# Kernel tuning notes

Hardware: AMD Instinct MI355X
Metric: run time of the kernel (lower is better)

## Reference

```python
import jax, jax.numpy as jnp
import numpy as np


def setup_inputs() -> dict:
    key = jax.random.key(0)
    ks = jax.random.split(key, 6)
    B, C_in, C_out, H, W = 4, 256, 128, 64, 64
    return {
        "p": jax.random.normal(ks[0], (B, C_in, H, W), dtype=jnp.float32),
        "b": jax.random.normal(ks[1], (B, C_in, H, W), dtype=jnp.float32),
        "Wq": jax.random.normal(ks[2], (C_out, C_in), dtype=jnp.float32) * 0.05,
        "bq": jax.random.normal(ks[3], (C_out,), dtype=jnp.float32) * 0.05,
        "Wk": jax.random.normal(ks[4], (C_out, C_in), dtype=jnp.float32) * 0.05,
        "bk": jax.random.normal(ks[5], (C_out,), dtype=jnp.float32) * 0.05,
    }


def reference(p, b, Wq, bq, Wk, bk):
    # p, b: [B, C, H, W]; 1x1 convs are per-pixel GEMMs over channels.
    B, C, H, W = p.shape
    N = H * W
    p_flat = p.reshape(B, C, N)  # [B, C, N]
    b_flat = b.reshape(B, C, N)  # [B, C, N]
    # query = Conv1x1(p) -> [B, O, N] -> permuted to [B, N, O]
    q = jnp.einsum("bcn,oc->bno", p_flat, Wq) + bq  # [B, N, O]
    # key = Conv1x1(b) -> [B, O, N]
    k = jnp.einsum("bcn,oc->bon", b_flat, Wk) + bk[:, None]  # [B, O, N]
    energy = jnp.einsum("bno,bom->bnm", q, k)  # [B, N, N]
    attention = jax.nn.softmax(energy, axis=-1)
    # value = b flattened, attention applied over spatial tokens
    out = jnp.einsum("bnm,bcm->bcn", attention, b_flat)  # [B, C, N]
    return out.reshape(B, C, H, W)
```

## Files before the change

### kernel.cpp

```cpp
#include <hip/hip_runtime.h>
#include <stdint.h>


#define B_ 4
#define C_ 256
#define O_ 128
#define N_ 4096

#define AP 72
#define PP 40

typedef float v4f __attribute__((ext_vector_type(4)));
typedef short v8s __attribute__((ext_vector_type(8)));
typedef _Float16 v8h __attribute__((ext_vector_type(8)));
typedef uint32_t u32;
typedef unsigned short u16;

__device__ __forceinline__ u16 bf16_rne(float f) {
  u32 u = __builtin_bit_cast(u32, f);
  u += 0x7fffu + ((u >> 16) & 1u);
  return (u16)(u >> 16);
}
__device__ __forceinline__ float bf16_f(u16 s) {
  u32 u = ((u32)s) << 16;
  return __builtin_bit_cast(float, u);
}
__device__ __forceinline__ u16 f16_rne(float f) {
  _Float16 h = (_Float16)f;
  return __builtin_bit_cast(u16, h);
}
__device__ __forceinline__ float f16_f(u16 s) {
  return (float)__builtin_bit_cast(_Float16, s);
}
__device__ __forceinline__ v4f mfma16(v8s a, v8s b, v4f c) {
  return __builtin_amdgcn_mfma_f32_16x16x32_bf16(a, b, c, 0, 0, 0);
}
__device__ __forceinline__ v4f mfma16h(v8h a, v8h b, v4f c) {
  return __builtin_amdgcn_mfma_f32_16x16x32_f16(a, b, c, 0, 0, 0);
}
__device__ __forceinline__ void gl16(const u16* g, u16* l) {
  __builtin_amdgcn_global_load_lds(
      (const __attribute__((address_space(1))) u32*)g,
      (__attribute__((address_space(3))) u32*)l, 16, 0, 0);
}
template <int CTRL>
__device__ __forceinline__ float dppadd(float x) {
  int yi = __builtin_amdgcn_update_dpp(0, __builtin_bit_cast(int, x), CTRL,
                                       0xf, 0xf, true);
  return x + __builtin_bit_cast(float, yi);
}
__device__ __forceinline__ float sum16(float x) {
  x = dppadd<0xB1>(x);
  x = dppadd<0x4E>(x);
  x = dppadd<0x141>(x);
  x = dppadd<0x140>(x);
  return x;
}

__global__ __launch_bounds__(256) void k_proj(
    const float* __restrict__ Xp, const float* __restrict__ Wq,
    const float* __restrict__ bq, const float* __restrict__ Xb,
    const float* __restrict__ Wk, const float* __restrict__ bk,
    u16* __restrict__ Qh, u16* __restrict__ Ql, u16* __restrict__ Kh,
    u16* __restrict__ Vbf) {
  __shared__ __align__(16) short ah[64 * AP];
  __shared__ __align__(16) short al[64 * AP];
  __shared__ __align__(16) short wh[128 * AP];
  __shared__ __align__(16) short wl[128 * AP];
  const int tid = threadIdx.x;
  const int inst = blockIdx.x >> 8;
  const float* X = inst ? Xb : Xp;
  const float* W = inst ? Wk : Wq;
  const float* bias = inst ? bk : bq;
  const int b = (blockIdx.x >> 6) & 3;
  const int n0 = (blockIdx.x & 63) << 6;
  const int w = tid >> 6, lane = tid & 63, l15 = lane & 15, quad = lane >> 4;
  v4f acc[8];
#pragma unroll
  for (int t = 0; t < 8; t++) acc[t] = (v4f){0.f, 0.f, 0.f, 0.f};

  for (int c0 = 0; c0 < C_; c0 += 64) {
    __syncthreads();
    {
      const int c = tid >> 2, nch = (tid & 3) << 4;
      const float* s = X + ((size_t)(b * C_ + c0 + c)) * N_ + n0 + nch;
      float4 f0 = ((const float4*)s)[0], f1 = ((const float4*)s)[1],
             f2 = ((const float4*)s)[2], f3 = ((const float4*)s)[3];
      float v[16] = {f0.x, f0.y, f0.z, f0.w, f1.x, f1.y, f1.z, f1.w,
                     f2.x, f2.y, f2.z, f2.w, f3.x, f3.y, f3.z, f3.w};
      u16 hh[16];
#pragma unroll
      for (int j = 0; j < 16; j++) {
        u16 h = bf16_rne(v[j]);
        u16 l = bf16_rne(v[j] - bf16_f(h));
        hh[j] = h;
        ah[(nch + j) * AP + c] = (short)h;
        al[(nch + j) * AP + c] = (short)l;
      }
      if (inst) {
        u32 pk[8];
#pragma unroll
        for (int jj = 0; jj < 8; jj++)
          pk[jj] = (u32)hh[2 * jj] | ((u32)hh[2 * jj + 1] << 16);
        u16* vd = Vbf + ((size_t)(b * C_ + c0 + c)) * N_ + n0 + nch;
        ((uint4*)vd)[0] = make_uint4(pk[0], pk[1], pk[2], pk[3]);
        ((uint4*)vd)[1] = make_uint4(pk[4], pk[5], pk[6], pk[7]);
      }
    }
    {
      const int o = tid >> 1, cch = (tid & 1) << 5;
      const float* s = W + (size_t)o * C_ + c0 + cch;
#pragma unroll
      for (int jj = 0; jj < 8; jj++) {
        float4 f = ((const float4*)s)[jj];
        float v[4] = {f.x, f.y, f.z, f.w};
#pragma unroll
        for (int j = 0; j < 4; j++) {
          u16 h = bf16_rne(v[j]);
          u16 l = bf16_rne(v[j] - bf16_f(h));
          wh[o * AP + cch + jj * 4 + j] = (short)h;
          wl[o * AP + cch + jj * 4 + j] = (short)l;
        }
      }
    }
    __syncthreads();
#pragma unroll
    for (int s = 0; s < 2; s++) {
      v8s a_h = *(const v8s*)&ah[(16 * w + l15) * AP + 32 * s + 8 * quad];
      v8s a_l = *(const v8s*)&al[(16 * w + l15) * AP + 32 * s + 8 * quad];
#pragma unroll
      for (int to = 0; to < 8; to++) {
        v8s b_h = *(const v8s*)&wh[(16 * to + l15) * AP + 32 * s + 8 * quad];
        v8s b_l = *(const v8s*)&wl[(16 * to + l15) * AP + 32 * s + 8 * quad];
        acc[to] = mfma16(a_h, b_h, acc[to]);
        acc[to] = mfma16(a_h, b_l, acc[to]);
        acc[to] = mfma16(a_l, b_h, acc[to]);
      }
    }
  }
#pragma unroll
  for (int to = 0; to < 8; to++) {
    const int o = 16 * to + l15;
    const float bv = bias[o];
#pragma unroll
    for (int r = 0; r < 4; r++) {
      const int n = n0 + 16 * w + 4 * quad + r;
      float v = acc[to][r] + bv;
      const size_t idx = (size_t)(b * N_ + n) * O_ + o;
      if (!inst) {
        u16 h = f16_rne(v);
        Qh[idx] = h;
        Ql[idx] = f16_rne(v - f16_f(h));
      } else {
        Kh[idx] = f16_rne(v);
      }
    }
  }
}

__global__ __launch_bounds__(256, 2) void k_flash(
    const u16* __restrict__ Qh, const u16* __restrict__ Ql,
    const u16* __restrict__ Khp, const u16* __restrict__ Vbf,
    u16* __restrict__ Opart, float* __restrict__ lpart) {
  __shared__ __align__(16) short smem[27136];
  short* Pt = smem + 24576;

  const int tid = threadIdx.x;
  const int w = tid >> 6, lane = tid & 63, l15 = lane & 15, quad = lane >> 4;
  const int h = blockIdx.x & 1;
  const int qt = (blockIdx.x >> 1) & 63;
  const int b = blockIdx.x >> 7;
  const int n0 = qt << 6;
  const int tok0 = h << 11;

  const u16* khb = Khp + (size_t)b * N_ * O_;
  const u16* vb = Vbf + (size_t)b * C_ * N_;

  v8h qh[4], ql[4];
  {
    const u16* qrh = Qh + (size_t)(b * N_ + n0 + 16 * w + l15) * O_;
    const u16* qrl = Ql + (size_t)(b * N_ + n0 + 16 * w + l15) * O_;
#pragma unroll
    for (int s = 0; s < 4; s++) {
      qh[s] = *(const v8h*)(qrh + 32 * s + 8 * quad);
      ql[s] = *(const v8h*)(qrl + 32 * s + 8 * quad);
    }
  }

  v4f oacc[16];
#pragma unroll
  for (int t = 0; t < 16; t++) oacc[t] = (v4f){0.f, 0.f, 0.f, 0.f};
  float lstate[4] = {0.f, 0.f, 0.f, 0.f};

  auto stage = [&](int mtn, int bi) {
    const int m0n = tok0 + (mtn << 5);
    short* kd = smem + bi * 12288;
    short* vd = kd + 4096;
#pragma unroll
    for (int i = 0; i < 2; i++) {
      const int R = 8 * w + 4 * i;
      const int rl = R + (lane >> 4);
      const int cg = (lane & 15) ^ (rl & 15);
      gl16(khb + ((size_t)(m0n + rl) << 7) + (cg << 3), (u16*)(kd + (R << 7)));
    }
#pragma unroll
    for (int i = 0; i < 4; i++) {
      const int R = 64 * w + 16 * i;
      const int rl = R + (lane >> 2);
      const int cg = (lane & 3) ^ ((rl >> 1) & 3);
      gl16(vb + (size_t)rl * N_ + m0n + (cg << 3), (u16*)(vd + (R << 5)));
    }
  };

  stage(0, 0);

#pragma unroll 1
  for (int mt = 0; mt < 64; mt++) {
    const int pr = mt & 1;
    __syncthreads();
    if (mt + 1 < 64) stage(mt + 1, 1 - pr);
    const short* kc = smem + pr * 12288;
    const short* vc = kc + 4096;

    v4f eh[2], el[2];
#pragma unroll
    for (int t = 0; t < 2; t++) {
      eh[t] = (v4f){0.f, 0.f, 0.f, 0.f};
      el[t] = (v4f){0.f, 0.f, 0.f, 0.f};
    }
#pragma unroll
    for (int s = 0; s < 4; s++) {
#pragma unroll
      for (int t = 0; t < 2; t++) {
        const int off = ((16 * t + l15) << 7) + (((4 * s + quad) ^ l15) << 3);
        const v8h kf = *(const v8h*)&kc[off];
        eh[t] = mfma16h(qh[s], kf, eh[t]);
        el[t] = mfma16h(ql[s], kf, el[t]);
      }
    }

#pragma unroll
    for (int r = 0; r < 4; r++) {
      float p0 = __expf(eh[0][r] + el[0][r]);
      float p1 = __expf(eh[1][r] + el[1][r]);
      lstate[r] += sum16(p0 + p1);
      Pt[(16 * w + 4 * quad + r) * PP + l15] = (short)bf16_rne(p0);
      Pt[(16 * w + 4 * quad + r) * PP + 16 + l15] = (short)bf16_rne(p1);
    }
    __builtin_amdgcn_s_waitcnt(0xC07F);
    asm volatile("s_barrier" ::: "memory");

    v8s af[4];
#pragma unroll
    for (int rw = 0; rw < 4; rw++)
      af[rw] = *(const v8s*)&Pt[(16 * rw + l15) * PP + 8 * quad];
#pragma unroll
    for (int cg = 0; cg < 4; cg++) {
      const int ch = 64 * w + 16 * cg + l15;
      const int voff = (ch << 5) + ((quad ^ ((ch >> 1) & 3)) << 3);
      const v8s vf = *(const v8s*)&vc[voff];
#pragma unroll
      for (int rw = 0; rw < 4; rw++)
        oacc[rw * 4 + cg] = mfma16(af[rw], vf, oacc[rw * 4 + cg]);
    }
  }

  __syncthreads();
  u16* outx = (u16*)smem;
#pragma unroll
  for (int rw = 0; rw < 4; rw++)
#pragma unroll
    for (int cg = 0; cg < 4; cg++) {
      const int ch = 64 * w + 16 * cg + l15;
      const v4f o = oacc[rw * 4 + cg];
      u32* q = (u32*)outx;
      const int base = ch * 36 + 8 * rw + 2 * quad;
      q[base] = (u32)bf16_rne(o[0]) | ((u32)bf16_rne(o[1]) << 16);
      q[base + 1] = (u32)bf16_rne(o[2]) | ((u32)bf16_rne(o[3]) << 16);
    }
  if (l15 == 0) {
#pragma unroll
    for (int r = 0; r < 4; r++)
      lpart[(size_t)blockIdx.x * 64 + 16 * w + 4 * quad + r] = lstate[r];
  }
  __syncthreads();
  {
    u16* od = Opart + (size_t)blockIdx.x * 16384;
    const int cr = tid >> 2, nch = (tid & 3) << 4;
#pragma unroll
    for (int it = 0; it < 4; it++) {
      const int c = cr + 64 * it;
      const u16* srcr = &outx[c * 72 + nch];
      uint4* dst = (uint4*)(od + c * 64 + nch);
      dst[0] = ((const uint4*)srcr)[0];
      dst[1] = ((const uint4*)srcr)[1];
    }
  }
}

__global__ __launch_bounds__(256) void k_merge(const u16* __restrict__ Opart,
                                               const float* __restrict__ lpart,
                                               float* __restrict__ out) {
  const int idx = blockIdx.x * 256 + threadIdx.x;
  const int e4 = idx << 2;
  const int b = e4 >> 20;
  const int c = (e4 >> 12) & 255;
  const int n = e4 & 4095;
  const int qt = n >> 6, row = n & 63;
  const int g = (b * 64 + qt) * 2;
  const u16* q0 = Opart + (size_t)g * 16384 + c * 64 + row;
  ushort4 a0 = *(const ushort4*)q0;
  ushort4 a1 = *(const ushort4*)(q0 + 16384);
  float4 l0 = *(const float4*)(lpart + (size_t)g * 64 + row);
  float4 l1 = *(const float4*)(lpart + (size_t)g * 64 + 64 + row);
  float4 o;
  o.x = (bf16_f(a0.x) + bf16_f(a1.x)) / (l0.x + l1.x);
  o.y = (bf16_f(a0.y) + bf16_f(a1.y)) / (l0.y + l1.y);
  o.z = (bf16_f(a0.z) + bf16_f(a1.z)) / (l0.z + l1.z);
  o.w = (bf16_f(a0.w) + bf16_f(a1.w)) / (l0.w + l1.w);
  *(float4*)(out + e4) = o;
}

extern "C" void kernel_launch(void* const* d_in, const int* in_sizes, int n_in,
                              void* d_out, int out_size, void* d_ws, size_t ws_size,
                              hipStream_t stream) {
  const float* p = (const float*)d_in[0];
  const float* bb = (const float*)d_in[1];
  const float* Wq = (const float*)d_in[2];
  const float* bq = (const float*)d_in[3];
  const float* Wk = (const float*)d_in[4];
  const float* bk = (const float*)d_in[5];
  float* out = (float*)d_out;

  const size_t plane = (size_t)B_ * N_ * O_;
  u16* Qh = (u16*)d_ws;
  u16* Ql = Qh + plane;
  u16* Kh = Ql + plane;
  u16* Vbf = Kh + plane;
  u16* Opart = Vbf + 2 * plane;
  float* lpart = (float*)(Opart + (size_t)512 * 16384);

  hipLaunchKernelGGL(k_proj, dim3(512), dim3(256), 0, stream, p, Wq, bq, bb,
                     Wk, bk, Qh, Ql, Kh, Vbf);
  hipLaunchKernelGGL(k_flash, dim3(B_ * 64 * 2), dim3(256), 0, stream, Qh, Ql,
                     Kh, Vbf, Opart, lpart);
  hipLaunchKernelGGL(k_merge, dim3((B_ * C_ * N_) / (256 * 4)), dim3(256), 0,
                     stream, Opart, lpart, out);
}
```

Baseline: 188.9 us.

## Split flash attention keys four ways and single-buffer V to raise occupancy

Splits the key dimension into four partitions instead of two, doubling the flash-kernel grid, and the merge kernel now combines four partial outputs. To fit more blocks per CU, V is now single-buffered while K stays double-buffered. This shrinks shared memory, and launch bounds now request 4 blocks per SM. The V load for the next tile is issued after the PV MFMAs behind an extra barrier, so V latency is less hidden and the partial-output traffic in the merge doubles.

```diff
diff --git a/kernel.cpp b/kernel.cpp
--- a/kernel.cpp
+++ b/kernel.cpp
@@ -158,20 +158,20 @@
   }
 }
 
-__global__ __launch_bounds__(256, 2) void k_flash(
+__global__ __launch_bounds__(256, 4) void k_flash(
     const u16* __restrict__ Qh, const u16* __restrict__ Ql,
     const u16* __restrict__ Khp, const u16* __restrict__ Vbf,
     u16* __restrict__ Opart, float* __restrict__ lpart) {
-  __shared__ __align__(16) short smem[27136];
-  short* Pt = smem + 24576;
+  __shared__ __align__(16) short smem[18944];
+  short* Pt = smem + 16384;
 
   const int tid = threadIdx.x;
   const int w = tid >> 6, lane = tid & 63, l15 = lane & 15, quad = lane >> 4;
-  const int h = blockIdx.x & 1;
-  const int qt = (blockIdx.x >> 1) & 63;
-  const int b = blockIdx.x >> 7;
+  const int h = blockIdx.x & 3;
+  const int qt = (blockIdx.x >> 2) & 63;
+  const int b = blockIdx.x >> 8;
   const int n0 = qt << 6;
-  const int tok0 = h << 11;
+  const int tok0 = h << 10;
 
   const u16* khb = Khp + (size_t)b * N_ * O_;
   const u16* vb = Vbf + (size_t)b * C_ * N_;
@@ -192,10 +192,9 @@
   for (int t = 0; t < 16; t++) oacc[t] = (v4f){0.f, 0.f, 0.f, 0.f};
   float lstate[4] = {0.f, 0.f, 0.f, 0.f};
 
-  auto stage = [&](int mtn, int bi) {
+  auto stageK = [&](int mtn, int bi) {
     const int m0n = tok0 + (mtn << 5);
-    short* kd = smem + bi * 12288;
-    short* vd = kd + 4096;
+    short* kd = smem + bi * 4096;
 #pragma unroll
     for (int i = 0; i < 2; i++) {
       const int R = 8 * w + 4 * i;
@@ -203,6 +202,10 @@
       const int cg = (lane & 15) ^ (rl & 15);
       gl16(khb + ((size_t)(m0n + rl) << 7) + (cg << 3), (u16*)(kd + (R << 7)));
     }
+  };
+  auto stageV = [&](int mtn) {
+    const int m0n = tok0 + (mtn << 5);
+    short* vd = smem + 8192;
 #pragma unroll
     for (int i = 0; i < 4; i++) {
       const int R = 64 * w + 16 * i;
@@ -212,15 +215,17 @@
     }
   };
 
-  stage(0, 0);
+  stageK(0, 0);
+  stageV(0);
 
 #pragma unroll 1
-  for (int mt = 0; mt < 64; mt++) {
+  for (int mt = 0; mt < 32; mt++) {
     const int pr = mt & 1;
-    __syncthreads();
-    if (mt + 1 < 64) stage(mt + 1, 1 - pr);
-    const short* kc = smem + pr * 12288;
-    const short* vc = kc + 4096;
+    __builtin_amdgcn_s_waitcnt(0x0F74);
+    asm volatile("s_barrier" ::: "memory");
+    if (mt + 1 < 32) stageK(mt + 1, 1 - pr);
+    const short* kc = smem + pr * 4096;
+    const short* vc = smem + 8192;
 
     v4f eh[2], el[2];
 #pragma unroll
@@ -247,7 +252,10 @@
       Pt[(16 * w + 4 * quad + r) * PP + l15] = (short)bf16_rne(p0);
       Pt[(16 * w + 4 * quad + r) * PP + 16 + l15] = (short)bf16_rne(p1);
     }
-    __builtin_amdgcn_s_waitcnt(0xC07F);
+    if (mt + 1 < 32)
+      __builtin_amdgcn_s_waitcnt(0x0072);
+    else
+      __builtin_amdgcn_s_waitcnt(0x0070);
     asm volatile("s_barrier" ::: "memory");
 
     v8s af[4];
@@ -263,6 +271,10 @@
       for (int rw = 0; rw < 4; rw++)
         oacc[rw * 4 + cg] = mfma16(af[rw], vf, oacc[rw * 4 + cg]);
     }
+
+    __builtin_amdgcn_s_waitcnt(0xC07F);
+    asm volatile("s_barrier" ::: "memory");
+    if (mt + 1 < 32) stageV(mt + 1);
   }
 
   __syncthreads();
@@ -307,17 +319,26 @@
   const int c = (e4 >> 12) & 255;
   const int n = e4 & 4095;
   const int qt = n >> 6, row = n & 63;
-  const int g = (b * 64 + qt) * 2;
+  const int g = (b * 64 + qt) * 4;
   const u16* q0 = Opart + (size_t)g * 16384 + c * 64 + row;
   ushort4 a0 = *(const ushort4*)q0;
   ushort4 a1 = *(const ushort4*)(q0 + 16384);
-  float4 l0 = *(const float4*)(lpart + (size_t)g * 64 + row);
-  float4 l1 = *(const float4*)(lpart + (size_t)g * 64 + 64 + row);
+  ushort4 a2 = *(const ushort4*)(q0 + 32768);
+  ushort4 a3 = *(const ushort4*)(q0 + 49152);
+  const float* lb = lpart + (size_t)g * 64 + row;
+  float4 l0 = *(const float4*)lb;
+  float4 l1 = *(const float4*)(lb + 64);
+  float4 l2 = *(const float4*)(lb + 128);
+  float4 l3 = *(const float4*)(lb + 192);
   float4 o;
-  o.x = (bf16_f(a0.x) + bf16_f(a1.x)) / (l0.x + l1.x);
-  o.y = (bf16_f(a0.y) + bf16_f(a1.y)) / (l0.y + l1.y);
-  o.z = (bf16_f(a0.z) + bf16_f(a1.z)) / (l0.z + l1.z);
-  o.w = (bf16_f(a0.w) + bf16_f(a1.w)) / (l0.w + l1.w);
+  o.x = (bf16_f(a0.x) + bf16_f(a1.x) + bf16_f(a2.x) + bf16_f(a3.x)) /
+        (l0.x + l1.x + l2.x + l3.x);
+  o.y = (bf16_f(a0.y) + bf16_f(a1.y) + bf16_f(a2.y) + bf16_f(a3.y)) /
+        (l0.y + l1.y + l2.y + l3.y);
+  o.z = (bf16_f(a0.z) + bf16_f(a1.z) + bf16_f(a2.z) + bf16_f(a3.z)) /
+        (l0.z + l1.z + l2.z + l3.z);
+  o.w = (bf16_f(a0.w) + bf16_f(a1.w) + bf16_f(a2.w) + bf16_f(a3.w)) /
+        (l0.w + l1.w + l2.w + l3.w);
   *(float4*)(out + e4) = o;
 }
 
@@ -338,11 +359,11 @@
   u16* Kh = Ql + plane;
   u16* Vbf = Kh + plane;
   u16* Opart = Vbf + 2 * plane;
-  float* lpart = (float*)(Opart + (size_t)512 * 16384);
+  float* lpart = (float*)(Opart + (size_t)1024 * 16384);
 
   hipLaunchKernelGGL(k_proj, dim3(512), dim3(256), 0, stream, p, Wq, bq, bb,
                      Wk, bk, Qh, Ql, Kh, Vbf);
-  hipLaunchKernelGGL(k_flash, dim3(B_ * 64 * 2), dim3(256), 0, stream, Qh, Ql,
+  hipLaunchKernelGGL(k_flash, dim3(B_ * 64 * 4), dim3(256), 0, stream, Qh, Ql,
                      Kh, Vbf, Opart, lpart);
   hipLaunchKernelGGL(k_merge, dim3((B_ * C_ * N_) / (256 * 4)), dim3(256), 0,
                      stream, Opart, lpart, out);
```

Measured after the change: 270.7 us. 1.43x slower.

## Restructure flash kernel to 8 waves with 64-key tiles and register-loaded V

Applied to the files above, without the earlier changes.

The attention kernel moves to 512-thread blocks and processes 64 keys per iteration. Wave halves split the QK tile between them, and each wave owns 32 output channels for the PV product. V fragments now load straight from global memory into registers instead of being staged in LDS, which frees shared memory. Block indices are remapped so the batch and split half follow the low bits of the block id, for cache locality across XCDs. Row sums are now stored per wave-half, so the merge adds four partial sums. The tighter launch bounds may cause register pressure or spills, and the unstaged V loads may expose global latency.

```diff
diff --git a/kernel.cpp b/kernel.cpp
--- a/kernel.cpp
+++ b/kernel.cpp
@@ -8,7 +8,7 @@
 #define N_ 4096
 
 #define AP 72
-#define PP 40
+#define PFP 72
 
 typedef float v4f __attribute__((ext_vector_type(4)));
 typedef short v8s __attribute__((ext_vector_type(8)));
@@ -158,28 +158,30 @@
   }
 }
 
-__global__ __launch_bounds__(256, 2) void k_flash(
+__global__ __launch_bounds__(512, 4) void k_flash(
     const u16* __restrict__ Qh, const u16* __restrict__ Ql,
     const u16* __restrict__ Khp, const u16* __restrict__ Vbf,
     u16* __restrict__ Opart, float* __restrict__ lpart) {
-  __shared__ __align__(16) short smem[27136];
-  short* Pt = smem + 24576;
+  __shared__ __align__(16) short smem[20992];
+  short* Pt = smem + 16384;
 
   const int tid = threadIdx.x;
   const int w = tid >> 6, lane = tid & 63, l15 = lane & 15, quad = lane >> 4;
-  const int h = blockIdx.x & 1;
-  const int qt = (blockIdx.x >> 1) & 63;
-  const int b = blockIdx.x >> 7;
+  const int wr = w & 3, wh2 = w >> 2;
+  const int xcd = blockIdx.x & 7;
+  const int b = xcd >> 1, h = xcd & 1;
+  const int qt = blockIdx.x >> 3;
   const int n0 = qt << 6;
   const int tok0 = h << 11;
+  const int og = (b << 7) + (qt << 1) + h;
 
   const u16* khb = Khp + (size_t)b * N_ * O_;
   const u16* vb = Vbf + (size_t)b * C_ * N_;
 
   v8h qh[4], ql[4];
   {
-    const u16* qrh = Qh + (size_t)(b * N_ + n0 + 16 * w + l15) * O_;
-    const u16* qrl = Ql + (size_t)(b * N_ + n0 + 16 * w + l15) * O_;
+    const u16* qrh = Qh + (size_t)(b * N_ + n0 + 16 * wr + l15) * O_;
+    const u16* qrl = Ql + (size_t)(b * N_ + n0 + 16 * wr + l15) * O_;
 #pragma unroll
     for (int s = 0; s < 4; s++) {
       qh[s] = *(const v8h*)(qrh + 32 * s + 8 * quad);
@@ -187,15 +189,14 @@
     }
   }
 
-  v4f oacc[16];
-#pragma unroll
-  for (int t = 0; t < 16; t++) oacc[t] = (v4f){0.f, 0.f, 0.f, 0.f};
+  v4f oacc[8];
+#pragma unroll
+  for (int t = 0; t < 8; t++) oacc[t] = (v4f){0.f, 0.f, 0.f, 0.f};
   float lstate[4] = {0.f, 0.f, 0.f, 0.f};
 
-  auto stage = [&](int mtn, int bi) {
-    const int m0n = tok0 + (mtn << 5);
-    short* kd = smem + bi * 12288;
-    short* vd = kd + 4096;
+  auto stageK = [&](int mtn, int bi) {
+    const int m0n = tok0 + (mtn << 6);
+    short* kd = smem + bi * 8192;
 #pragma unroll
     for (int i = 0; i < 2; i++) {
       const int R = 8 * w + 4 * i;
@@ -203,24 +204,28 @@
       const int cg = (lane & 15) ^ (rl & 15);
       gl16(khb + ((size_t)(m0n + rl) << 7) + (cg << 3), (u16*)(kd + (R << 7)));
     }
-#pragma unroll
-    for (int i = 0; i < 4; i++) {
-      const int R = 64 * w + 16 * i;
-      const int rl = R + (lane >> 2);
-      const int cg = (lane & 3) ^ ((rl >> 1) & 3);
-      gl16(vb + (size_t)rl * N_ + m0n + (cg << 3), (u16*)(vd + (R << 5)));
-    }
   };
 
-  stage(0, 0);
+  stageK(0, 0);
+
+  const u16* vrow = vb + (size_t)(32 * w + l15) * N_ + (quad << 3);
 
 #pragma unroll 1
-  for (int mt = 0; mt < 64; mt++) {
+  for (int mt = 0; mt < 32; mt++) {
     const int pr = mt & 1;
+    const int m0 = tok0 + (mt << 6);
     __syncthreads();
-    if (mt + 1 < 64) stage(mt + 1, 1 - pr);
-    const short* kc = smem + pr * 12288;
-    const short* vc = kc + 4096;
+
+    v8s vfr[2][2];
+#pragma unroll
+    for (int cg = 0; cg < 2; cg++)
+#pragma unroll
+      for (int s = 0; s < 2; s++)
+        vfr[cg][s] =
+            *(const v8s*)(vrow + (size_t)(cg << 4) * N_ + m0 + (s << 5));
+
+    if (mt + 1 < 32) stageK(mt + 1, 1 - pr);
+    const short* kc = smem + pr * 8192;
 
     v4f eh[2], el[2];
 #pragma unroll
@@ -232,7 +237,8 @@
     for (int s = 0; s < 4; s++) {
 #pragma unroll
       for (int t = 0; t < 2; t++) {
-        const int off = ((16 * t + l15) << 7) + (((4 * s + quad) ^ l15) << 3);
+        const int row = (wh2 << 5) + (t << 4) + l15;
+        const int off = (row << 7) + (((4 * s + quad) ^ l15) << 3);
         const v8h kf = *(const v8h*)&kc[off];
         eh[t] = mfma16h(qh[s], kf, eh[t]);
         el[t] = mfma16h(ql[s], kf, el[t]);
@@ -244,24 +250,25 @@
       float p0 = __expf(eh[0][r] + el[0][r]);
       float p1 = __expf(eh[1][r] + el[1][r]);
       lstate[r] += sum16(p0 + p1);
-      Pt[(16 * w + 4 * quad + r) * PP + l15] = (short)bf16_rne(p0);
-      Pt[(16 * w + 4 * quad + r) * PP + 16 + l15] = (short)bf16_rne(p1);
+      const int prow = ((wr << 4) + 4 * quad + r) * PFP + (wh2 << 5);
+      Pt[prow + l15] = (short)bf16_rne(p0);
+      Pt[prow + 16 + l15] = (short)bf16_rne(p1);
     }
     __builtin_amdgcn_s_waitcnt(0xC07F);
     asm volatile("s_barrier" ::: "memory");
 
-    v8s af[4];
-#pragma unroll
-    for (int rw = 0; rw < 4; rw++)
-      af[rw] = *(const v8s*)&Pt[(16 * rw + l15) * PP + 8 * quad];
-#pragma unroll
-    for (int cg = 0; cg < 4; cg++) {
-      const int ch = 64 * w + 16 * cg + l15;
-      const int voff = (ch << 5) + ((quad ^ ((ch >> 1) & 3)) << 3);
-      const v8s vf = *(const v8s*)&vc[voff];
+#pragma unroll
+    for (int s = 0; s < 2; s++) {
+      v8s af[4];
 #pragma unroll
       for (int rw = 0; rw < 4; rw++)
-        oacc[rw * 4 + cg] = mfma16(af[rw], vf, oacc[rw * 4 + cg]);
+        af[rw] =
+            *(const v8s*)&Pt[((rw << 4) + l15) * PFP + (s << 5) + (quad << 3)];
+#pragma unroll
+      for (int cg = 0; cg < 2; cg++)
+#pragma unroll
+        for (int rw = 0; rw < 4; rw++)
+          oacc[rw * 2 + cg] = mfma16(af[rw], vfr[cg][s], oacc[rw * 2 + cg]);
     }
   }
 
@@ -270,30 +277,28 @@
 #pragma unroll
   for (int rw = 0; rw < 4; rw++)
 #pragma unroll
-    for (int cg = 0; cg < 4; cg++) {
-      const int ch = 64 * w + 16 * cg + l15;
-      const v4f o = oacc[rw * 4 + cg];
+    for (int cg = 0; cg < 2; cg++) {
+      const int ch = (w << 5) + (cg << 4) + l15;
+      const v4f o = oacc[rw * 2 + cg];
       u32* q = (u32*)outx;
-      const int base = ch * 36 + 8 * rw + 2 * quad;
+      const int base = ch * 36 + (rw << 3) + (quad << 1);
       q[base] = (u32)bf16_rne(o[0]) | ((u32)bf16_rne(o[1]) << 16);
       q[base + 1] = (u32)bf16_rne(o[2]) | ((u32)bf16_rne(o[3]) << 16);
     }
   if (l15 == 0) {
 #pragma unroll
     for (int r = 0; r < 4; r++)
-      lpart[(size_t)blockIdx.x * 64 + 16 * w + 4 * quad + r] = lstate[r];
+      lpart[(size_t)og * 128 + (wh2 << 6) + (wr << 4) + 4 * quad + r] =
+          lstate[r];
   }
   __syncthreads();
   {
-    u16* od = Opart + (size_t)blockIdx.x * 16384;
-    const int cr = tid >> 2, nch = (tid & 3) << 4;
+    u16* od = Opart + (size_t)og * 16384;
+    const int cr = tid >> 3, col = (tid & 7) << 3;
 #pragma unroll
     for (int it = 0; it < 4; it++) {
       const int c = cr + 64 * it;
-      const u16* srcr = &outx[c * 72 + nch];
-      uint4* dst = (uint4*)(od + c * 64 + nch);
-      dst[0] = ((const uint4*)srcr)[0];
-      dst[1] = ((const uint4*)srcr)[1];
+      *(uint4*)(od + c * 64 + col) = *(const uint4*)&outx[c * 72 + col];
     }
   }
 }
@@ -307,17 +312,20 @@
   const int c = (e4 >> 12) & 255;
   const int n = e4 & 4095;
   const int qt = n >> 6, row = n & 63;
-  const int g = (b * 64 + qt) * 2;
-  const u16* q0 = Opart + (size_t)g * 16384 + c * 64 + row;
+  const int g2 = (b << 7) + (qt << 1);
+  const u16* q0 = Opart + (size_t)g2 * 16384 + c * 64 + row;
   ushort4 a0 = *(const ushort4*)q0;
   ushort4 a1 = *(const ushort4*)(q0 + 16384);
-  float4 l0 = *(const float4*)(lpart + (size_t)g * 64 + row);
-  float4 l1 = *(const float4*)(lpart + (size_t)g * 64 + 64 + row);
+  const float* lb = lpart + (size_t)g2 * 128 + row;
+  float4 l0 = *(const float4*)lb;
+  float4 l1 = *(const float4*)(lb + 64);
+  float4 l2 = *(const float4*)(lb + 128);
+  float4 l3 = *(const float4*)(lb + 192);
   float4 o;
-  o.x = (bf16_f(a0.x) + bf16_f(a1.x)) / (l0.x + l1.x);
-  o.y = (bf16_f(a0.y) + bf16_f(a1.y)) / (l0.y + l1.y);
-  o.z = (bf16_f(a0.z) + bf16_f(a1.z)) / (l0.z + l1.z);
-  o.w = (bf16_f(a0.w) + bf16_f(a1.w)) / (l0.w + l1.w);
+  o.x = (bf16_f(a0.x) + bf16_f(a1.x)) / (l0.x + l1.x + l2.x + l3.x);
+  o.y = (bf16_f(a0.y) + bf16_f(a1.y)) / (l0.y + l1.y + l2.y + l3.y);
+  o.z = (bf16_f(a0.z) + bf16_f(a1.z)) / (l0.z + l1.z + l2.z + l3.z);
+  o.w = (bf16_f(a0.w) + bf16_f(a1.w)) / (l0.w + l1.w + l2.w + l3.w);
   *(float4*)(out + e4) = o;
 }
 
@@ -342,7 +350,7 @@
 
   hipLaunchKernelGGL(k_proj, dim3(512), dim3(256), 0, stream, p, Wq, bq, bb,
                      Wk, bk, Qh, Ql, Kh, Vbf);
-  hipLaunchKernelGGL(k_flash, dim3(B_ * 64 * 2), dim3(256), 0, stream, Qh, Ql,
+  hipLaunchKernelGGL(k_flash, dim3(B_ * 64 * 2), dim3(512), 0, stream, Qh, Ql,
                      Kh, Vbf, Opart, lpart);
   hipLaunchKernelGGL(k_merge, dim3((B_ * C_ * N_) / (256 * 4)), dim3(256), 0,
                      stream, Opart, lpart, out);
```

New measurement: 193.4 us. 2.4% more time.
